# Kernel tuning notes

Hardware: AMD Instinct MI355X
Metric: run time of the kernel (lower is better)

## Reference

```python
import jax, jax.numpy as jnp
import numpy as np


def setup_inputs() -> dict:
    key = jax.random.key(0)
    kx, kq, kk, kv = jax.random.split(key, 4)
    d_model, d_head = 1024, 64
    x = jax.random.normal(kx, (4, 4096, d_model), dtype=jnp.float32)
    scale = 1.0 / np.sqrt(d_model)
    Wq = jax.random.normal(kq, (d_model, d_head), dtype=jnp.float32) * scale
    Wk = jax.random.normal(kk, (d_model, d_head), dtype=jnp.float32) * scale
    Wv = jax.random.normal(kv, (d_model, d_head), dtype=jnp.float32) * scale
    return {"x": x, "Wq": Wq, "Wk": Wk, "Wv": Wv}


def reference(x, Wq, Wk, Wv):
    # x: [B, S, D]; Wq/Wk/Wv: [D, H]
    d_head = Wq.shape[-1]
    Q = jnp.einsum('bsd,dh->bsh', x, Wq)
    K = jnp.einsum('bsd,dh->bsh', x, Wk)
    V = jnp.einsum('bsd,dh->bsh', x, Wv)
    scores = jnp.einsum('bqh,bkh->bqk', Q, K) / jnp.sqrt(jnp.float32(d_head))
    S = x.shape[1]
    causal = jnp.tril(jnp.ones((S, S), dtype=bool))  # [S, S]
    scores = jnp.where(causal, scores, -jnp.inf)
    weights = jax.nn.softmax(scores, axis=-1)  # [B, S, S]
    return jnp.einsum('bqk,bkh->bqh', weights, V)
```

## Files before the change

### kernel.cpp

```cpp
#include <hip/hip_runtime.h>

#define D_MODEL 1024
#define D_HEAD  64
#define SEQ     4096
#define BATCH   4
#define M_TOT   (BATCH * SEQ)
#define LOG2E   1.44269504088896f
#define MFIX_L2 17.3123404906676f
#define CHUNK   16

typedef __bf16 bf16;
typedef bf16  bf16x8 __attribute__((ext_vector_type(8)));
typedef bf16  bf16x4v __attribute__((ext_vector_type(4)));
typedef float f32x4  __attribute__((ext_vector_type(4)));

#define MFMA(a, b, c) __builtin_amdgcn_mfma_f32_16x16x32_bf16(a, b, c, 0, 0, 0)

#define WAIT_BARRIER(N) do {                                       \
    __builtin_amdgcn_sched_barrier(0);                             \
    asm volatile("s_waitcnt vmcnt(" #N ")" ::: "memory");          \
    __builtin_amdgcn_s_barrier();                                  \
    __builtin_amdgcn_sched_barrier(0);                             \
} while (0)

__device__ __forceinline__ void gld16(const void* g, void* l) {
    __builtin_amdgcn_global_load_lds(
        (const __attribute__((address_space(1))) void*)g,
        (__attribute__((address_space(3))) void*)l, 16, 0, 0);
}

#define QKV_OFF  0
#define OBUF_OFF 6291456
#define LBUF_OFF 10485760
#define WT_OFF   10551296
#define VT_OFF   10944512

__global__ void prep_kernel(const float* __restrict__ Wq, const float* __restrict__ Wk,
                            const float* __restrict__ Wv, bf16* __restrict__ Wt,
                            float4* __restrict__ zp, int n4)
{
    const int bx = blockIdx.x;
    const int t  = threadIdx.x;
    if (bx < 48) {
        __shared__ bf16 tr[64][72];
        const int wm = bx >> 4, kt = bx & 15, k0 = kt * 64;
        const float* W = (wm == 0) ? Wq : (wm == 1) ? Wk : Wv;
        const int kr = t >> 2, nb = (t & 3) * 16;
        #pragma unroll
        for (int j = 0; j < 4; j++) {
            float4 wrow = *(const float4*)(W + (size_t)(k0 + kr) * D_HEAD + nb + j * 4);
            tr[nb + j * 4 + 0][kr] = (bf16)wrow.x;
            tr[nb + j * 4 + 1][kr] = (bf16)wrow.y;
            tr[nb + j * 4 + 2][kr] = (bf16)wrow.z;
            tr[nb + j * 4 + 3][kr] = (bf16)wrow.w;
        }
        __syncthreads();
        const int n = t >> 2, kc = (t & 3) * 8;
        bf16* dst = Wt + (size_t)(wm * 64 + n) * D_MODEL + k0;
        #pragma unroll
        for (int h = 0; h < 2; h++) {
            bf16x8 v;
            #pragma unroll
            for (int j = 0; j < 8; j++) v[j] = tr[n][kc + h * 32 + j];
            *(bf16x8*)(dst + kc + h * 32) = v;
        }
    } else {
        int i = (bx - 48) * 256 + t;
        if (i < n4) zp[i] = float4{0.f, 0.f, 0.f, 0.f};
    }
}

__global__ __launch_bounds__(512, 1) void proj_kernel(
    const float* __restrict__ x, const bf16* __restrict__ Wt,
    bf16* __restrict__ qkv, bf16* __restrict__ vt)
{
    __shared__ __align__(16) char Al[3][64 * 256];
    __shared__ __align__(16) char Bl[3][192 * 128];

    const int t    = threadIdx.x;
    const int w    = t >> 6;
    const int rg2  = w >> 2;
    const int nw   = w & 3;
    const int lane = t & 63;
    const int quad = lane >> 4;
    const int l15  = lane & 15;
    const int row0 = blockIdx.x * 64;

    const char* xb = (const char*)x;
    const char* wb = (const char*)Wt;

    f32x4 acc[6] = {};

    auto stageA = [&](int bsel, int step) {
        #pragma unroll
        for (int i = 0; i < 2; i++) {
            const int s  = w * 2 + i;
            const int r  = s * 4 + (lane >> 4);
            const int cs = ((lane & 15) * 16) ^ ((r & 7) << 4);
            gld16(xb + (size_t)(row0 + r) * 4096 + step * 256 + cs,
                  (char*)Al[bsel] + s * 1024);
        }
    };
    auto stageB = [&](int bsel, int step) {
        #pragma unroll
        for (int i = 0; i < 3; i++) {
            const int s  = w * 3 + i;
            const int n  = s * 8 + (lane >> 3);
            const int cs = ((lane & 7) * 16) ^ ((n & 7) << 4);
            gld16(wb + (size_t)n * 2048 + step * 128 + cs,
                  (char*)Bl[bsel] + s * 1024);
        }
    };

    auto cvt8 = [](float4 lo, float4 hi) {
        bf16x8 r;
        r[0] = (bf16)lo.x; r[1] = (bf16)lo.y; r[2] = (bf16)lo.z; r[3] = (bf16)lo.w;
        r[4] = (bf16)hi.x; r[5] = (bf16)hi.y; r[6] = (bf16)hi.z; r[7] = (bf16)hi.w;
        return r;
    };

    auto compute = [&](int bsel) {
        const char* Ab = Al[bsel];
        const char* Bb = Bl[bsel];
        #pragma unroll
        for (int ks = 0; ks < 2; ks++) {
            bf16x8 afr[2];
            #pragma unroll
            for (int rg = 0; rg < 2; rg++) {
                const int r  = rg2 * 32 + rg * 16 + l15;
                const int o  = ks * 128 + quad * 32;
                const int m  = (r & 7) << 4;
                float4 lo = *(const float4*)(Ab + r * 256 + (o ^ m));
                float4 hi = *(const float4*)(Ab + r * 256 + ((o + 16) ^ m));
                afr[rg] = cvt8(lo, hi);
            }
            #pragma unroll
            for (int j = 0; j < 3; j++) {
                const int n  = nw * 48 + j * 16 + l15;
                const int o  = ks * 64 + quad * 16;
                bf16x8 bfrg = *(const bf16x8*)(Bb + n * 128 + (o ^ ((n & 7) << 4)));
                acc[j]     = MFMA(afr[0], bfrg, acc[j]);
                acc[3 + j] = MFMA(afr[1], bfrg, acc[3 + j]);
            }
        }
    };

    stageA(0, 0); stageB(0, 0);
    stageA(1, 1); stageB(1, 1);

    int buf = 0;
    for (int s = 0; s < 16; s++) {
        if (s + 1 < 16) { WAIT_BARRIER(5); }
        else            { WAIT_BARRIER(0); }
        if (s + 2 < 16) {
            int nb2 = buf + 2; if (nb2 >= 3) nb2 -= 3;
            stageA(nb2, s + 2); stageB(nb2, s + 2);
        }
        compute(buf);
        buf = (buf == 2) ? 0 : buf + 1;
    }

    const int bb = row0 >> 12, s0v = row0 & (SEQ - 1);
    const int rbase = rg2 * 32;
    #pragma unroll
    for (int rg = 0; rg < 2; rg++)
        #pragma unroll
        for (int j = 0; j < 3; j++) {
            const int col = nw * 48 + j * 16 + l15;
            const int wm = col >> 6, h = col & 63;
            if (wm == 2) {
                bf16x4v vv;
                #pragma unroll
                for (int r = 0; r < 4; r++)
                    vv[r] = (bf16)acc[rg * 3 + j][r];
                *(bf16x4v*)(vt + ((size_t)bb * D_HEAD + h) * SEQ +
                            s0v + rbase + rg * 16 + quad * 4) = vv;
            } else {
                const float sc = (wm == 0) ? 0.125f : 1.0f;
                bf16* outp = qkv + (size_t)wm * M_TOT * D_HEAD;
                #pragma unroll
                for (int r = 0; r < 4; r++) {
                    const int row = row0 + rbase + rg * 16 + quad * 4 + r;
                    outp[(size_t)row * D_HEAD + h] =
                        (bf16)(acc[rg * 3 + j][r] * sc);
                }
            }
        }
}

__global__ __launch_bounds__(256, 3) void attn_kernel(
    const bf16* __restrict__ qkv, const bf16* __restrict__ vt,
    float* __restrict__ o_buf, float* __restrict__ l_buf)
{
    const int i = blockIdx.x;
    const int c = blockIdx.y;
    const int b = blockIdx.z;
    const int ntiles = i + 1;
    const int tile0  = c * CHUNK;
    if (tile0 >= ntiles) return;
    const int tile1 = min(tile0 + CHUNK, ntiles);

    __shared__ __align__(16) char KsB[3 * 64 * 128];
    __shared__ __align__(16) char VsB[3 * 64 * 128];

    auto kaddr = [](char* base, int pp, int row, int colb) -> void* {
        return base + pp * 8192 + row * 128 + (colb ^ ((row & 7) << 4));
    };

    const bf16* Q = qkv;
    const bf16* K = qkv + (size_t)M_TOT * D_HEAD;

    const int t    = threadIdx.x;
    const int wv   = t >> 6;
    const int lane = t & 63;
    const int quad = lane >> 4;
    const int l15  = lane & 15;
    const int qb   = i * 64;
    const size_t base  = (size_t)b * SEQ * D_HEAD;
    const bf16* vtb = vt + (size_t)b * D_HEAD * SEQ;

    bf16x8 qf0, qf1;
    {
        const bf16* qr = Q + base + (size_t)(qb + wv * 16 + l15) * D_HEAD;
        qf0 = *(const bf16x8*)(qr + quad * 8);
        qf1 = *(const bf16x8*)(qr + 32 + quad * 8);
    }

    f32x4 o[4] = {};
    float lsum = 0.f;
    const int qw0 = qb + wv * 16;

    const char* Kb = (const char*)(K + base);
    const char* Vb = (const char*)vtb;

    auto stage_kv = [&](int tile, int pp) {
        #pragma unroll
        for (int i2 = 0; i2 < 2; i2++) {
            const int s  = wv * 2 + i2;
            const int rr = s * 8 + (lane >> 3);
            const int sw = ((lane & 7) * 16) ^ ((lane >> 3) << 4);
            gld16(Kb + (size_t)(tile * 64 + rr) * 128 + sw,
                  KsB + pp * 8192 + s * 1024);
            gld16(Vb + (size_t)rr * (SEQ * 2) + (size_t)tile * 128 + sw,
                  VsB + pp * 8192 + s * 1024);
        }
    };

    stage_kv(tile0, 0);
    if (tile0 + 1 < tile1) stage_kv(tile0 + 1, 1);

    int p = 0;
    for (int tile = tile0; tile < tile1; tile++) {
        const int kk0 = tile * 64;

        if (tile + 1 < tile1) { WAIT_BARRIER(4); }
        else                  { WAIT_BARRIER(0); }

        if (tile + 2 < tile1) {
            int nb2 = p + 2; if (nb2 >= 3) nb2 -= 3;
            stage_kv(tile + 2, nb2);
        }

        f32x4 sc4[4];
        __builtin_amdgcn_s_setprio(1);
        #pragma unroll
        for (int kt = 0; kt < 4; kt++) {
            f32x4 z = {};
            z = MFMA(*(bf16x8*)kaddr(KsB, p, kt * 16 + l15, quad * 16),      qf0, z);
            z = MFMA(*(bf16x8*)kaddr(KsB, p, kt * 16 + l15, 64 + quad * 16), qf1, z);
            sc4[kt] = z;
        }
        __builtin_amdgcn_s_setprio(0);

        bf16 ph[4][4];
        if (tile == i) {
            #pragma unroll
            for (int kt = 0; kt < 4; kt++)
                #pragma unroll
                for (int r = 0; r < 4; r++) {
                    float s = sc4[kt][r];
                    if (kk0 + kt * 16 + quad * 4 + r > qw0 + l15)
                        s = -1e30f;
                    float pe = __builtin_amdgcn_exp2f(fmaf(s, LOG2E, -MFIX_L2));
                    lsum += pe;
                    ph[kt][r] = (bf16)pe;
                }
        } else {
            #pragma unroll
            for (int kt = 0; kt < 4; kt++)
                #pragma unroll
                for (int r = 0; r < 4; r++) {
                    float pe = __builtin_amdgcn_exp2f(
                        fmaf(sc4[kt][r], LOG2E, -MFIX_L2));
                    lsum += pe;
                    ph[kt][r] = (bf16)pe;
                }
        }

        unsigned pku[4][2];
        #pragma unroll
        for (int kt = 0; kt < 4; kt++) {
            __builtin_memcpy(&pku[kt][0], &ph[kt][0], 4);
            __builtin_memcpy(&pku[kt][1], &ph[kt][2], 4);
        }

        const int srcA = l15 + ((lane & 16) ? 32 : 0);
        const int srcB = srcA + 16;
        const bool hi  = (lane & 32) != 0;

        #pragma unroll
        for (int c2 = 0; c2 < 2; c2++) {
            unsigned xA0 = __shfl((int)pku[2 * c2][0],     srcA);
            unsigned xA1 = __shfl((int)pku[2 * c2][1],     srcA);
            unsigned yA0 = __shfl((int)pku[2 * c2 + 1][0], srcA);
            unsigned yA1 = __shfl((int)pku[2 * c2 + 1][1], srcA);
            unsigned xB0 = __shfl((int)pku[2 * c2][0],     srcB);
            unsigned xB1 = __shfl((int)pku[2 * c2][1],     srcB);
            unsigned yB0 = __shfl((int)pku[2 * c2 + 1][0], srcB);
            unsigned yB1 = __shfl((int)pku[2 * c2 + 1][1], srcB);
            unsigned fr[4];
            fr[0] = hi ? yA0 : xA0;
            fr[1] = hi ? yA1 : xA1;
            fr[2] = hi ? yB0 : xB0;
            fr[3] = hi ? yB1 : xB1;
            bf16x8 pa;
            __builtin_memcpy(&pa, fr, 16);

            __builtin_amdgcn_s_setprio(1);
            #pragma unroll
            for (int t4 = 0; t4 < 4; t4++) {
                bf16x8 vb = *(bf16x8*)kaddr(VsB, p, t4 * 16 + l15,
                                            c2 * 64 + quad * 16);
                o[t4] = MFMA(pa, vb, o[t4]);
            }
            __builtin_amdgcn_s_setprio(0);
        }

        p = (p == 2) ? 0 : p + 1;
    }

    const int mrow0 = b * SEQ + qw0;
    lsum += __shfl_xor(lsum, 16, 64);
    lsum += __shfl_xor(lsum, 32, 64);
    if (lane < 16)
        atomicAdd(&l_buf[mrow0 + l15], lsum);
    #pragma unroll
    for (int r = 0; r < 4; r++) {
        const size_t orow = (size_t)(mrow0 + quad * 4 + r) * D_HEAD;
        #pragma unroll
        for (int t4 = 0; t4 < 4; t4++)
            atomicAdd(&o_buf[orow + t4 * 16 + l15], o[t4][r]);
    }
}

__global__ void norm_kernel(const float4* __restrict__ o_buf,
                            const float* __restrict__ l_buf,
                            float4* __restrict__ out)
{
    int gid = blockIdx.x * 256 + threadIdx.x;
    int m = gid >> 4;
    float inv = 1.0f / l_buf[m];
    float4 v = o_buf[gid];
    out[gid] = float4{v.x * inv, v.y * inv, v.z * inv, v.w * inv};
}

extern "C" void kernel_launch(void* const* d_in, const int* in_sizes, int n_in,
                              void* d_out, int out_size, void* d_ws, size_t ws_size,
                              hipStream_t stream) {
    const float* x  = (const float*)d_in[0];
    const float* Wq = (const float*)d_in[1];
    const float* Wk = (const float*)d_in[2];
    const float* Wv = (const float*)d_in[3];

    bf16*  qkv   = (bf16*)((char*)d_ws + QKV_OFF);
    float* o_buf = (float*)((char*)d_ws + OBUF_OFF);
    float* l_buf = (float*)((char*)d_ws + LBUF_OFF);
    bf16*  Wt    = (bf16*)((char*)d_ws + WT_OFF);
    bf16*  vt    = (bf16*)((char*)d_ws + VT_OFF);

    const int zero4 = (M_TOT * 65) / 4;
    const int zblocks = (zero4 + 255) / 256;
    prep_kernel<<<48 + zblocks, 256, 0, stream>>>(Wq, Wk, Wv, Wt,
                                                  (float4*)o_buf, zero4);
    proj_kernel<<<M_TOT / 64, 512, 0, stream>>>(x, Wt, qkv, vt);
    attn_kernel<<<dim3(SEQ / 64, SEQ / 64 / CHUNK, BATCH), 256, 0, stream>>>(
        qkv, vt, o_buf, l_buf);
    norm_kernel<<<M_TOT * 16 / 256, 256, 0, stream>>>((const float4*)o_buf, l_buf,
                                                      (float4*)d_out);
}
```

Baseline: 149.7 us.

## Drop split-KV chunking and fuse normalization into the attention kernel

Each attention block now walks the full causal key range for its 64-row query tile, instead of splitting keys into 16-tile chunks across extra grid blocks. Because every row is owned by one block, the atomic accumulation into global O/L buffers goes away, along with the zeroing pass in the prep kernel and the separate normalization kernel. Rows are divided by their softmax sum and written straight to the output. The trade-off is far less parallelism and a long, unbalanced critical path: the grid drops to 256 blocks and the last query tiles must each process 64 key tiles serially.

After: 185.7 us. 24.1% more time.

```diff
diff --git a/kernel.cpp b/kernel.cpp
--- a/kernel.cpp
+++ b/kernel.cpp
@@ -7,7 +7,6 @@
 #define M_TOT   (BATCH * SEQ)
 #define LOG2E   1.44269504088896f
 #define MFIX_L2 17.3123404906676f
-#define CHUNK   16
 
 typedef __bf16 bf16;
 typedef bf16  bf16x8 __attribute__((ext_vector_type(8)));
@@ -30,43 +29,35 @@
 }
 
 #define QKV_OFF  0
-#define OBUF_OFF 6291456
-#define LBUF_OFF 10485760
 #define WT_OFF   10551296
 #define VT_OFF   10944512
 
 __global__ void prep_kernel(const float* __restrict__ Wq, const float* __restrict__ Wk,
-                            const float* __restrict__ Wv, bf16* __restrict__ Wt,
-                            float4* __restrict__ zp, int n4)
+                            const float* __restrict__ Wv, bf16* __restrict__ Wt)
 {
+    __shared__ bf16 tr[64][72];
     const int bx = blockIdx.x;
     const int t  = threadIdx.x;
-    if (bx < 48) {
-        __shared__ bf16 tr[64][72];
-        const int wm = bx >> 4, kt = bx & 15, k0 = kt * 64;
-        const float* W = (wm == 0) ? Wq : (wm == 1) ? Wk : Wv;
-        const int kr = t >> 2, nb = (t & 3) * 16;
-        #pragma unroll
-        for (int j = 0; j < 4; j++) {
-            float4 wrow = *(const float4*)(W + (size_t)(k0 + kr) * D_HEAD + nb + j * 4);
-            tr[nb + j * 4 + 0][kr] = (bf16)wrow.x;
-            tr[nb + j * 4 + 1][kr] = (bf16)wrow.y;
-            tr[nb + j * 4 + 2][kr] = (bf16)wrow.z;
-            tr[nb + j * 4 + 3][kr] = (bf16)wrow.w;
-        }
-        __syncthreads();
-        const int n = t >> 2, kc = (t & 3) * 8;
-        bf16* dst = Wt + (size_t)(wm * 64 + n) * D_MODEL + k0;
-        #pragma unroll
-        for (int h = 0; h < 2; h++) {
-            bf16x8 v;
-            #pragma unroll
-            for (int j = 0; j < 8; j++) v[j] = tr[n][kc + h * 32 + j];
-            *(bf16x8*)(dst + kc + h * 32) = v;
-        }
-    } else {
-        int i = (bx - 48) * 256 + t;
-        if (i < n4) zp[i] = float4{0.f, 0.f, 0.f, 0.f};
+    const int wm = bx >> 4, kt = bx & 15, k0 = kt * 64;
+    const float* W = (wm == 0) ? Wq : (wm == 1) ? Wk : Wv;
+    const int kr = t >> 2, nb = (t & 3) * 16;
+    #pragma unroll
+    for (int j = 0; j < 4; j++) {
+        float4 wrow = *(const float4*)(W + (size_t)(k0 + kr) * D_HEAD + nb + j * 4);
+        tr[nb + j * 4 + 0][kr] = (bf16)wrow.x;
+        tr[nb + j * 4 + 1][kr] = (bf16)wrow.y;
+        tr[nb + j * 4 + 2][kr] = (bf16)wrow.z;
+        tr[nb + j * 4 + 3][kr] = (bf16)wrow.w;
+    }
+    __syncthreads();
+    const int n = t >> 2, kc = (t & 3) * 8;
+    bf16* dst = Wt + (size_t)(wm * 64 + n) * D_MODEL + k0;
+    #pragma unroll
+    for (int h = 0; h < 2; h++) {
+        bf16x8 v;
+        #pragma unroll
+        for (int j = 0; j < 8; j++) v[j] = tr[n][kc + h * 32 + j];
+        *(bf16x8*)(dst + kc + h * 32) = v;
     }
 }
 
@@ -190,15 +181,11 @@
 
 __global__ __launch_bounds__(256, 3) void attn_kernel(
     const bf16* __restrict__ qkv, const bf16* __restrict__ vt,
-    float* __restrict__ o_buf, float* __restrict__ l_buf)
+    float* __restrict__ out)
 {
     const int i = blockIdx.x;
-    const int c = blockIdx.y;
-    const int b = blockIdx.z;
+    const int b = blockIdx.y;
     const int ntiles = i + 1;
-    const int tile0  = c * CHUNK;
-    if (tile0 >= ntiles) return;
-    const int tile1 = min(tile0 + CHUNK, ntiles);
 
     __shared__ __align__(16) char KsB[3 * 64 * 128];
     __shared__ __align__(16) char VsB[3 * 64 * 128];
@@ -246,17 +233,17 @@
         }
     };
 
-    stage_kv(tile0, 0);
-    if (tile0 + 1 < tile1) stage_kv(tile0 + 1, 1);
+    stage_kv(0, 0);
+    if (1 < ntiles) stage_kv(1, 1);
 
     int p = 0;
-    for (int tile = tile0; tile < tile1; tile++) {
+    for (int tile = 0; tile < ntiles; tile++) {
         const int kk0 = tile * 64;
 
-        if (tile + 1 < tile1) { WAIT_BARRIER(4); }
-        else                  { WAIT_BARRIER(0); }
-
-        if (tile + 2 < tile1) {
+        if (tile + 1 < ntiles) { WAIT_BARRIER(4); }
+        else                   { WAIT_BARRIER(0); }
+
+        if (tile + 2 < ntiles) {
             int nb2 = p + 2; if (nb2 >= 3) nb2 -= 3;
             stage_kv(tile + 2, nb2);
         }
@@ -339,29 +326,18 @@
         p = (p == 2) ? 0 : p + 1;
     }
 
-    const int mrow0 = b * SEQ + qw0;
     lsum += __shfl_xor(lsum, 16, 64);
     lsum += __shfl_xor(lsum, 32, 64);
-    if (lane < 16)
-        atomicAdd(&l_buf[mrow0 + l15], lsum);
+    float* outp = out + (size_t)(b * SEQ + qw0) * D_HEAD;
     #pragma unroll
     for (int r = 0; r < 4; r++) {
-        const size_t orow = (size_t)(mrow0 + quad * 4 + r) * D_HEAD;
+        float lr  = __shfl(lsum, quad * 4 + r, 64);
+        float inv = 1.0f / lr;
+        float* orow = outp + (size_t)(quad * 4 + r) * D_HEAD;
         #pragma unroll
         for (int t4 = 0; t4 < 4; t4++)
-            atomicAdd(&o_buf[orow + t4 * 16 + l15], o[t4][r]);
-    }
-}
-
-__global__ void norm_kernel(const float4* __restrict__ o_buf,
-                            const float* __restrict__ l_buf,
-                            float4* __restrict__ out)
-{
-    int gid = blockIdx.x * 256 + threadIdx.x;
-    int m = gid >> 4;
-    float inv = 1.0f / l_buf[m];
-    float4 v = o_buf[gid];
-    out[gid] = float4{v.x * inv, v.y * inv, v.z * inv, v.w * inv};
+            orow[t4 * 16 + l15] = o[t4][r] * inv;
+    }
 }
 
 extern "C" void kernel_launch(void* const* d_in, const int* in_sizes, int n_in,
@@ -373,18 +349,11 @@
     const float* Wv = (const float*)d_in[3];
 
     bf16*  qkv   = (bf16*)((char*)d_ws + QKV_OFF);
-    float* o_buf = (float*)((char*)d_ws + OBUF_OFF);
-    float* l_buf = (float*)((char*)d_ws + LBUF_OFF);
     bf16*  Wt    = (bf16*)((char*)d_ws + WT_OFF);
     bf16*  vt    = (bf16*)((char*)d_ws + VT_OFF);
 
-    const int zero4 = (M_TOT * 65) / 4;
-    const int zblocks = (zero4 + 255) / 256;
-    prep_kernel<<<48 + zblocks, 256, 0, stream>>>(Wq, Wk, Wv, Wt,
-                                                  (float4*)o_buf, zero4);
+    prep_kernel<<<48, 256, 0, stream>>>(Wq, Wk, Wv, Wt);
     proj_kernel<<<M_TOT / 64, 512, 0, stream>>>(x, Wt, qkv, vt);
-    attn_kernel<<<dim3(SEQ / 64, SEQ / 64 / CHUNK, BATCH), 256, 0, stream>>>(
-        qkv, vt, o_buf, l_buf);
-    norm_kernel<<<M_TOT * 16 / 256, 256, 0, stream>>>((const float4*)o_buf, l_buf,
-                                                      (float4*)d_out);
-}
+    attn_kernel<<<dim3(SEQ / 64, BATCH), 256, 0, stream>>>(qkv, vt,
+                                                           (float*)d_out);
+}
```
